# Kernel optimization log

Hardware: AMD Instinct MI355X
Metric: run time of the kernel (lower is better)

Reference implementation:

```python
import jax, jax.numpy as jnp
import numpy as np

N = 50000
E = 800000
F_IN = 128
HID = 32
C = 16


def setup_inputs() -> dict:
    key = jax.random.key(0)
    ks = jax.random.split(key, 8)
    x = jax.random.normal(ks[0], (N, F_IN), dtype=jnp.float32)
    edge_index = jax.random.randint(ks[1], (2, E), 0, N, dtype=jnp.int64)
    edge_attr = jax.random.uniform(ks[2], (E,), dtype=jnp.float32)
    W_rel1 = jax.random.normal(ks[3], (F_IN, HID), dtype=jnp.float32) / np.sqrt(F_IN)
    W_root1 = jax.random.normal(ks[4], (F_IN, HID), dtype=jnp.float32) / np.sqrt(F_IN)
    b1 = jnp.zeros((HID,), dtype=jnp.float32)
    W_rel2 = jax.random.normal(ks[5], (HID, C), dtype=jnp.float32) / np.sqrt(HID)
    W_root2 = jax.random.normal(ks[6], (HID, C), dtype=jnp.float32) / np.sqrt(HID)
    b2 = jnp.zeros((C,), dtype=jnp.float32)
    return {"x": x, "edge_index": edge_index, "edge_attr": edge_attr,
            "W_rel1": W_rel1, "W_root1": W_root1, "b1": b1,
            "W_rel2": W_rel2, "W_root2": W_root2, "b2": b2}


def reference(x, edge_index, edge_attr, W_rel1, W_root1, b1, W_rel2, W_root2, b2):
    src = edge_index[0]  # message source (x_j)
    dst = edge_index[1]  # aggregation target

    def graph_conv(h, W_rel, W_root, b):
        # PyG GraphConv: out = lin_rel(sum_{j in N(i)} w_ij * h_j) + lin_root(h_i)
        msg = h[src] * edge_attr[:, None]                       # [E, d]
        agg = jax.ops.segment_sum(msg, dst, num_segments=h.shape[0])  # [N, d]
        return agg @ W_rel + h @ W_root + b

    h = jax.nn.relu(graph_conv(x, W_rel1, W_root1, b1))          # [N, 32]
    out = graph_conv(h, W_rel2, W_root2, b2)                     # [N, C]
    return jax.nn.log_softmax(out, axis=1)
```

## Files before the change

### kernel.cpp

```cpp
#include <hip/hip_runtime.h>
#include <math.h>

#define N_NODES 50000
#define E_EDGES 800000
#define F_INDIM 128
#define HID 32
#define C_OUT 16

#define BSH 6
#define BNODE 64
#define NB 782
#define BCAP 1280
#define BINA_BLKS 128
#define CH 6250

#define K1ROWS 128
#define K1PAD 136
#define KC 32
#define K1BLKS 391

typedef unsigned long long u64;
typedef unsigned short ushort_t;

__device__ __forceinline__ ushort_t bf16rne(float f) {
    unsigned u = __float_as_uint(f);
    return (ushort_t)((u + 0x7FFFu + ((u >> 16) & 1u)) >> 16);
}
__device__ __forceinline__ float bf16tof(ushort_t b) {
    return __uint_as_float((unsigned)b << 16);
}

__global__ __launch_bounds__(512) void k_fuseA(
        const float* __restrict__ x,
        const float* __restrict__ Wrel, const float* __restrict__ Wroot,
        const float* __restrict__ b1,
        const int* __restrict__ ei, const float* __restrict__ ea,
        int* __restrict__ bcur, u64* __restrict__ arena,
        ushort_t* __restrict__ t1b, ushort_t* __restrict__ t2c) {
    __shared__ __align__(16) char smem[25600];
    const int tid = threadIdx.x;

    if (blockIdx.x < BINA_BLKS) {
        int* hist = (int*)smem;
        int* cur  = hist + NB;
        int* gb   = cur + NB;
        const int e0 = blockIdx.x * CH;

        for (int i = tid; i < NB; i += 512) hist[i] = 0;
        __syncthreads();
        for (int k = tid; k < CH; k += 512)
            atomicAdd(&hist[ei[E_EDGES + e0 + k] >> BSH], 1);
        __syncthreads();
        for (int i = tid; i < NB; i += 512) {
            int b = i + blockIdx.x; if (b >= NB) b -= NB;
            int cnt = hist[b];
            gb[b] = b * BCAP + (cnt ? atomicAdd(&bcur[b], cnt) : 0);
            cur[b] = 0;
        }
        __syncthreads();
        for (int k = tid; k < CH; k += 512) {
            int e = e0 + k;
            int src = ei[e];
            int dst = ei[E_EDGES + e];
            float w = ea[e];
            int bkt = dst >> BSH;
            int p = atomicAdd(&cur[bkt], 1);
            unsigned lo = (unsigned)src | ((unsigned)(dst & (BNODE - 1)) << 16);
            arena[(size_t)gb[bkt] + p] = (u64)lo | ((u64)__float_as_uint(w) << 32);
        }
    } else {
        float (*sW)[64] = (float(*)[64])smem;
        float (*sxT)[K1PAD] = (float(*)[K1PAD])(smem + 8192);
        const int rowBase = (blockIdx.x - BINA_BLKS) * K1ROWS;
        const int c = tid & 31;
        const int g = tid >> 5;
        const float4* x4 = (const float4*)x;

        float acc1[8], acc2[8];
#pragma unroll
        for (int i = 0; i < 8; ++i) { acc1[i] = 0.f; acc2[i] = 0.f; }

        for (int kc = 0; kc < F_INDIM / KC; ++kc) {
            const int k0 = kc * KC;
            for (int i = tid; i < KC * 64; i += 512) {
                int k = i >> 6, j = i & 63;
                int cc = j >> 1, m = j & 1;
                sW[k][j] = m ? Wroot[(k0 + k) * HID + cc]
                             : Wrel[(k0 + k) * HID + cc];
            }
            for (int i = tid; i < K1ROWS * (KC / 4); i += 512) {
                int r = i >> 3, q = i & 7;
                int row = rowBase + r;
                float4 v = make_float4(0.f, 0.f, 0.f, 0.f);
                if (row < N_NODES) v = x4[(size_t)row * 32 + (k0 >> 2) + q];
                sxT[4 * q + 0][r] = v.x;
                sxT[4 * q + 1][r] = v.y;
                sxT[4 * q + 2][r] = v.z;
                sxT[4 * q + 3][r] = v.w;
            }
            __syncthreads();
#pragma unroll 4
            for (int k = 0; k < KC; ++k) {
                float2 w = *(const float2*)&sW[k][2 * c];
                float4 xa = *(const float4*)&sxT[k][8 * g];
                float4 xb = *(const float4*)&sxT[k][8 * g + 4];
                acc1[0] = fmaf(xa.x, w.x, acc1[0]); acc2[0] = fmaf(xa.x, w.y, acc2[0]);
                acc1[1] = fmaf(xa.y, w.x, acc1[1]); acc2[1] = fmaf(xa.y, w.y, acc2[1]);
                acc1[2] = fmaf(xa.z, w.x, acc1[2]); acc2[2] = fmaf(xa.z, w.y, acc2[2]);
                acc1[3] = fmaf(xa.w, w.x, acc1[3]); acc2[3] = fmaf(xa.w, w.y, acc2[3]);
                acc1[4] = fmaf(xb.x, w.x, acc1[4]); acc2[4] = fmaf(xb.x, w.y, acc2[4]);
                acc1[5] = fmaf(xb.y, w.x, acc1[5]); acc2[5] = fmaf(xb.y, w.y, acc2[5]);
                acc1[6] = fmaf(xb.z, w.x, acc1[6]); acc2[6] = fmaf(xb.z, w.y, acc2[6]);
                acc1[7] = fmaf(xb.w, w.x, acc1[7]); acc2[7] = fmaf(xb.w, w.y, acc2[7]);
            }
            __syncthreads();
        }

        const float bc = b1[c];
#pragma unroll
        for (int i = 0; i < 8; ++i) {
            int row = rowBase + 8 * g + i;
            if (row < N_NODES) {
                t1b[(size_t)row * HID + c] = bf16rne(acc1[i]);
                t2c[(size_t)row * HID + c] = bf16rne(acc2[i] + bc);
            }
        }
    }
}

__global__ __launch_bounds__(256) void k_binB(const int* __restrict__ bcur,
                                              const u64* __restrict__ arena,
                                              unsigned* __restrict__ erec,
                                              int* __restrict__ rowptr) {
    __shared__ int cur[BNODE];
    __shared__ int hist[BNODE];
    __shared__ int sbase;
    const int tid = threadIdx.x;
    const int b = blockIdx.x;
    if (tid < 64) {
        int acc = 0;
        for (int i = tid; i < b; i += 64) acc += bcur[i];
#pragma unroll
        for (int d = 1; d < 64; d <<= 1) acc += __shfl_xor(acc, d);
        if (tid == 0) sbase = acc;
    }
    if (tid < BNODE) hist[tid] = 0;
    __syncthreads();
    const int cnt = bcur[b];
    const u64* seg = arena + (size_t)b * BCAP;
    for (int i = tid; i < cnt; i += 256)
        atomicAdd(&hist[((unsigned)seg[i] >> 16) & (BNODE - 1)], 1);
    __syncthreads();
    if (tid < 64) {
        int v = hist[tid];
        int inc = v;
#pragma unroll
        for (int d = 1; d < 64; d <<= 1) {
            int t = __shfl_up(inc, d);
            if (tid >= d) inc += t;
        }
        int ex = inc - v;
        cur[tid] = ex;
        int node = (b << BSH) + tid;
        if (node < N_NODES) rowptr[node] = sbase + ex;
    }
    if (b == NB - 1 && tid == 0) rowptr[N_NODES] = E_EDGES;
    __syncthreads();
    const int gbase = sbase;
    for (int i = tid; i < cnt; i += 256) {
        u64 r = seg[i];
        unsigned lo = (unsigned)r;
        int dl = (lo >> 16) & (BNODE - 1);
        int p = atomicAdd(&cur[dl], 1);
        unsigned wu = (unsigned)(r >> 32);
        unsigned wb = (wu + 0x7FFFu + ((wu >> 16) & 1u)) & 0xFFFF0000u;
        erec[gbase + p] = wb | (lo & 0xFFFFu);
    }
}

__global__ __launch_bounds__(256) void k_gather1(
        const int* __restrict__ rowptr, const unsigned* __restrict__ erec,
        const ushort_t* __restrict__ t1b, const ushort_t* __restrict__ t2c,
        const float* __restrict__ Wrel2, const float* __restrict__ Wroot2,
        const float* __restrict__ b2,
        ushort_t* __restrict__ u1b, float* __restrict__ u2b) {
    __shared__ float hbuf[4][HID];
    const int tid = threadIdx.x;
    const int lane = tid & 63;
    const int wid = tid >> 6;

    const int node = blockIdx.x * 4 + wid;
    const int start = rowptr[node];
    const int end = rowptr[node + 1];

    const int er2 = lane >> 5;
    const int j = lane & 31;
    const float* Wsel = (j < 16) ? (Wrel2 + (j & 15)) : (Wroot2 + (j & 15));
    float w2r[16];
#pragma unroll
    for (int kk = 0; kk < 16; ++kk)
        w2r[kk] = Wsel[(er2 * 16 + kk) * C_OUT];

    const int er = lane >> 3;
    const int c4 = lane & 7;
    float ax = 0.f, ay = 0.f, az = 0.f, aw = 0.f;
    float bx = 0.f, by = 0.f, bz = 0.f, bw = 0.f;
    int e = start + er;
    for (; e + 8 < end; e += 16) {
        unsigned r0 = erec[e];
        unsigned r1 = erec[e + 8];
        float w0 = __uint_as_float(r0 & 0xFFFF0000u);
        float w1 = __uint_as_float(r1 & 0xFFFF0000u);
        ushort4 p0 = *(const ushort4*)&t1b[(size_t)(r0 & 0xFFFFu) * HID + 4 * c4];
        ushort4 p1 = *(const ushort4*)&t1b[(size_t)(r1 & 0xFFFFu) * HID + 4 * c4];
        ax = fmaf(w0, bf16tof(p0.x), ax); ay = fmaf(w0, bf16tof(p0.y), ay);
        az = fmaf(w0, bf16tof(p0.z), az); aw = fmaf(w0, bf16tof(p0.w), aw);
        bx = fmaf(w1, bf16tof(p1.x), bx); by = fmaf(w1, bf16tof(p1.y), by);
        bz = fmaf(w1, bf16tof(p1.z), bz); bw = fmaf(w1, bf16tof(p1.w), bw);
    }
    if (e < end) {
        unsigned r0 = erec[e];
        float w0 = __uint_as_float(r0 & 0xFFFF0000u);
        ushort4 p0 = *(const ushort4*)&t1b[(size_t)(r0 & 0xFFFFu) * HID + 4 * c4];
        ax = fmaf(w0, bf16tof(p0.x), ax); ay = fmaf(w0, bf16tof(p0.y), ay);
        az = fmaf(w0, bf16tof(p0.z), az); aw = fmaf(w0, bf16tof(p0.w), aw);
    }
    ax += bx; ay += by; az += bz; aw += bw;
#pragma unroll
    for (int d = 8; d < 64; d <<= 1) {
        ax += __shfl_xor(ax, d);
        ay += __shfl_xor(ay, d);
        az += __shfl_xor(az, d);
        aw += __shfl_xor(aw, d);
    }
    ushort4 t2u = *(const ushort4*)&t2c[(size_t)node * HID + 4 * c4];
    float4 hv;
    hv.x = ax + bf16tof(t2u.x); hv.x = hv.x > 0.f ? hv.x : 0.f;
    hv.y = ay + bf16tof(t2u.y); hv.y = hv.y > 0.f ? hv.y : 0.f;
    hv.z = az + bf16tof(t2u.z); hv.z = hv.z > 0.f ? hv.z : 0.f;
    hv.w = aw + bf16tof(t2u.w); hv.w = hv.w > 0.f ? hv.w : 0.f;
    if (er == 0) *(float4*)&hbuf[wid][4 * c4] = hv;
    __syncthreads();

    float outv = 0.f;
#pragma unroll
    for (int kk = 0; kk < 16; ++kk)
        outv = fmaf(hbuf[wid][er2 * 16 + kk], w2r[kk], outv);
    outv += __shfl_xor(outv, 32);
    if (er2 == 0) {
        int cc = j & 15;
        if (j < 16) u1b[(size_t)node * C_OUT + cc] = bf16rne(outv);
        else        u2b[(size_t)node * C_OUT + cc] = outv + b2[cc];
    }
}

__global__ __launch_bounds__(256) void k_gather2(
        const int* __restrict__ rowptr, const unsigned* __restrict__ erec,
        const ushort_t* __restrict__ u1b, const float* __restrict__ u2b,
        float* __restrict__ out) {
    const int tid = threadIdx.x;
    const int lane = tid & 63;
    const int node = blockIdx.x * 4 + (tid >> 6);
    const int start = rowptr[node];
    const int end = rowptr[node + 1];
    const int er = lane >> 3;
    const int c2 = lane & 7;
    float a0x = 0.f, a0y = 0.f, a1x = 0.f, a1y = 0.f;
    int e = start + er;
    for (; e + 8 < end; e += 16) {
        unsigned r0 = erec[e];
        unsigned r1 = erec[e + 8];
        float w0 = __uint_as_float(r0 & 0xFFFF0000u);
        float w1 = __uint_as_float(r1 & 0xFFFF0000u);
        ushort2 p0 = *(const ushort2*)&u1b[(size_t)(r0 & 0xFFFFu) * C_OUT + 2 * c2];
        ushort2 p1 = *(const ushort2*)&u1b[(size_t)(r1 & 0xFFFFu) * C_OUT + 2 * c2];
        a0x = fmaf(w0, bf16tof(p0.x), a0x);
        a0y = fmaf(w0, bf16tof(p0.y), a0y);
        a1x = fmaf(w1, bf16tof(p1.x), a1x);
        a1y = fmaf(w1, bf16tof(p1.y), a1y);
    }
    if (e < end) {
        unsigned r0 = erec[e];
        float w0 = __uint_as_float(r0 & 0xFFFF0000u);
        ushort2 p0 = *(const ushort2*)&u1b[(size_t)(r0 & 0xFFFFu) * C_OUT + 2 * c2];
        a0x = fmaf(w0, bf16tof(p0.x), a0x);
        a0y = fmaf(w0, bf16tof(p0.y), a0y);
    }
    float ax = a0x + a1x;
    float ay = a0y + a1y;
    ax += __shfl_xor(ax, 8);  ay += __shfl_xor(ay, 8);
    ax += __shfl_xor(ax, 16); ay += __shfl_xor(ay, 16);
    ax += __shfl_xor(ax, 32); ay += __shfl_xor(ay, 32);
    float2 u2 = *(const float2*)&u2b[(size_t)node * C_OUT + 2 * c2];
    float vx = ax + u2.x;
    float vy = ay + u2.y;
    float mx = fmaxf(vx, vy);
#pragma unroll
    for (int d = 1; d < 8; d <<= 1) mx = fmaxf(mx, __shfl_xor(mx, d));
    float s = expf(vx - mx) + expf(vy - mx);
#pragma unroll
    for (int d = 1; d < 8; d <<= 1) s += __shfl_xor(s, d);
    float lse = mx + logf(s);
    if (er == 0)
        *(float2*)&out[(size_t)node * C_OUT + 2 * c2] = make_float2(vx - lse, vy - lse);
}

extern "C" void kernel_launch(void* const* d_in, const int* in_sizes, int n_in,
                              void* d_out, int out_size, void* d_ws, size_t ws_size,
                              hipStream_t stream) {
    const float* x      = (const float*)d_in[0];
    const int*   ei     = (const int*)d_in[1];
    const float* ea     = (const float*)d_in[2];
    const float* Wrel1  = (const float*)d_in[3];
    const float* Wroot1 = (const float*)d_in[4];
    const float* b1     = (const float*)d_in[5];
    const float* Wrel2  = (const float*)d_in[6];
    const float* Wroot2 = (const float*)d_in[7];
    const float* b2     = (const float*)d_in[8];
    float* out = (float*)d_out;

    float* ws = (float*)d_ws;
    float*    u2b  = ws;
    ushort_t* t1b  = (ushort_t*)(ws + 800000);
    ushort_t* t2c  = (ushort_t*)(ws + 1600000);
    ushort_t* u1b  = (ushort_t*)(ws + 2400000);
    u64*      arena = (u64*)(ws + 2600000);
    unsigned* erec = (unsigned*)(ws + 2600000 + (size_t)NB * BCAP * 2);
    int*      bcur   = (int*)(erec + E_EDGES);
    int*      rowptr = bcur + NB;

    (void)hipMemsetAsync(bcur, 0, NB * sizeof(int), stream);
    k_fuseA<<<BINA_BLKS + K1BLKS, 512, 0, stream>>>(
        x, Wrel1, Wroot1, b1, ei, ea, bcur, arena, t1b, t2c);
    k_binB<<<NB, 256, 0, stream>>>(bcur, arena, erec, rowptr);
    k_gather1<<<N_NODES / 4, 256, 0, stream>>>(
        rowptr, erec, t1b, t2c, Wrel2, Wroot2, b2, u1b, u2b);
    k_gather2<<<N_NODES / 4, 256, 0, stream>>>(rowptr, erec, u1b, u2b, out);
}
```

Baseline: 88.54 us.

## Fuse bin pass B into the first kernel using a global completion flag

Merges the second binning kernel into the fused first kernel as extra blocks. These blocks spin on a global counter until every bin-A block has signalled completion, then each one processes two buckets with its 512 threads. This removes one kernel launch and its boundary, and lets bin-B work overlap the dense GEMM blocks. It relies on the bin-A blocks being scheduled before or alongside the spinning blocks, so forward progress depends on block dispatch order, and spinning blocks can occupy CU slots.

After: 172.2 us. +94.5%, slower.

```diff
diff --git a/kernel.cpp b/kernel.cpp
--- a/kernel.cpp
+++ b/kernel.cpp
@@ -18,6 +18,8 @@
 #define K1PAD 136
 #define KC 32
 #define K1BLKS 391
+#define BINB_BLKS 391
+#define MEGA_BLKS (BINA_BLKS + K1BLKS + BINB_BLKS)
 
 typedef unsigned long long u64;
 typedef unsigned short ushort_t;
@@ -30,13 +32,15 @@
     return __uint_as_float((unsigned)b << 16);
 }
 
-__global__ __launch_bounds__(512) void k_fuseA(
+__global__ __launch_bounds__(512) void k_mega(
         const float* __restrict__ x,
         const float* __restrict__ Wrel, const float* __restrict__ Wroot,
         const float* __restrict__ b1,
         const int* __restrict__ ei, const float* __restrict__ ea,
-        int* __restrict__ bcur, u64* __restrict__ arena,
-        ushort_t* __restrict__ t1b, ushort_t* __restrict__ t2c) {
+        int* __restrict__ bcur, int* __restrict__ dflag,
+        u64* __restrict__ arena,
+        ushort_t* __restrict__ t1b, ushort_t* __restrict__ t2c,
+        unsigned* __restrict__ erec, int* __restrict__ rowptr) {
     __shared__ __align__(16) char smem[25600];
     const int tid = threadIdx.x;
 
@@ -68,7 +72,12 @@
             unsigned lo = (unsigned)src | ((unsigned)(dst & (BNODE - 1)) << 16);
             arena[(size_t)gb[bkt] + p] = (u64)lo | ((u64)__float_as_uint(w) << 32);
         }
-    } else {
+        __syncthreads();
+        if (tid == 0) {
+            __threadfence();
+            atomicAdd(dflag, 1);
+        }
+    } else if (blockIdx.x < BINA_BLKS + K1BLKS) {
         float (*sW)[64] = (float(*)[64])smem;
         float (*sxT)[K1PAD] = (float(*)[K1PAD])(smem + 8192);
         const int rowBase = (blockIdx.x - BINA_BLKS) * K1ROWS;
@@ -125,56 +134,62 @@
                 t2c[(size_t)row * HID + c] = bf16rne(acc2[i] + bc);
             }
         }
-    }
-}
-
-__global__ __launch_bounds__(256) void k_binB(const int* __restrict__ bcur,
-                                              const u64* __restrict__ arena,
-                                              unsigned* __restrict__ erec,
-                                              int* __restrict__ rowptr) {
-    __shared__ int cur[BNODE];
-    __shared__ int hist[BNODE];
-    __shared__ int sbase;
-    const int tid = threadIdx.x;
-    const int b = blockIdx.x;
-    if (tid < 64) {
-        int acc = 0;
-        for (int i = tid; i < b; i += 64) acc += bcur[i];
-#pragma unroll
-        for (int d = 1; d < 64; d <<= 1) acc += __shfl_xor(acc, d);
-        if (tid == 0) sbase = acc;
-    }
-    if (tid < BNODE) hist[tid] = 0;
-    __syncthreads();
-    const int cnt = bcur[b];
-    const u64* seg = arena + (size_t)b * BCAP;
-    for (int i = tid; i < cnt; i += 256)
-        atomicAdd(&hist[((unsigned)seg[i] >> 16) & (BNODE - 1)], 1);
-    __syncthreads();
-    if (tid < 64) {
-        int v = hist[tid];
-        int inc = v;
-#pragma unroll
-        for (int d = 1; d < 64; d <<= 1) {
-            int t = __shfl_up(inc, d);
-            if (tid >= d) inc += t;
-        }
-        int ex = inc - v;
-        cur[tid] = ex;
-        int node = (b << BSH) + tid;
-        if (node < N_NODES) rowptr[node] = sbase + ex;
-    }
-    if (b == NB - 1 && tid == 0) rowptr[N_NODES] = E_EDGES;
-    __syncthreads();
-    const int gbase = sbase;
-    for (int i = tid; i < cnt; i += 256) {
-        u64 r = seg[i];
-        unsigned lo = (unsigned)r;
-        int dl = (lo >> 16) & (BNODE - 1);
-        int p = atomicAdd(&cur[dl], 1);
-        unsigned wu = (unsigned)(r >> 32);
-        unsigned wb = (wu + 0x7FFFu + ((wu >> 16) & 1u)) & 0xFFFF0000u;
-        erec[gbase + p] = wb | (lo & 0xFFFFu);
+    } else {
+        int* hist2 = (int*)smem;
+        int* cur2  = hist2 + 2 * BNODE;
+        int* base2 = cur2 + 2 * BNODE;
+        if (tid == 0) {
+            while (atomicAdd(dflag, 0) < BINA_BLKS)
+                __builtin_amdgcn_s_sleep(2);
+        }
+        __syncthreads();
+        __threadfence();
+
+        const int half = tid >> 8;
+        const int ltid = tid & 255;
+        const int b = (blockIdx.x - (BINA_BLKS + K1BLKS)) * 2 + half;
+        int* hist = hist2 + half * BNODE;
+        int* cur  = cur2 + half * BNODE;
+
+        if (ltid < 64) {
+            int acc = 0;
+            for (int i = ltid; i < b; i += 64) acc += bcur[i];
+#pragma unroll
+            for (int d = 1; d < 64; d <<= 1) acc += __shfl_xor(acc, d);
+            if (ltid == 0) base2[half] = acc;
+        }
+        if (ltid < BNODE) hist[ltid] = 0;
+        __syncthreads();
+        const int cnt = bcur[b];
+        const u64* seg = arena + (size_t)b * BCAP;
+        for (int i = ltid; i < cnt; i += 256)
+            atomicAdd(&hist[((unsigned)seg[i] >> 16) & (BNODE - 1)], 1);
+        __syncthreads();
+        if (ltid < 64) {
+            int v = hist[ltid];
+            int inc = v;
+#pragma unroll
+            for (int d = 1; d < 64; d <<= 1) {
+                int t = __shfl_up(inc, d);
+                if (ltid >= d) inc += t;
+            }
+            int ex = inc - v;
+            cur[ltid] = ex;
+            int node = (b << BSH) + ltid;
+            if (node < N_NODES) rowptr[node] = base2[half] + ex;
+        }
+        if (b == NB - 1 && ltid == 0) rowptr[N_NODES] = E_EDGES;
+        __syncthreads();
+        const int gbase = base2[half];
+        for (int i = ltid; i < cnt; i += 256) {
+            u64 r = seg[i];
+            unsigned lo = (unsigned)r;
+            int dl = (lo >> 16) & (BNODE - 1);
+            int p = atomicAdd(&cur[dl], 1);
+            unsigned wu = (unsigned)(r >> 32);
+            unsigned wb = (wu + 0x7FFFu + ((wu >> 16) & 1u)) & 0xFFFF0000u;
+            erec[gbase + p] = wb | (lo & 0xFFFFu);
+        }
     }
 }
 
@@ -327,12 +342,12 @@
     u64*      arena = (u64*)(ws + 2600000);
     unsigned* erec = (unsigned*)(ws + 2600000 + (size_t)NB * BCAP * 2);
     int*      bcur   = (int*)(erec + E_EDGES);
-    int*      rowptr = bcur + NB;
-
-    (void)hipMemsetAsync(bcur, 0, NB * sizeof(int), stream);
-    k_fuseA<<<BINA_BLKS + K1BLKS, 512, 0, stream>>>(
-        x, Wrel1, Wroot1, b1, ei, ea, bcur, arena, t1b, t2c);
-    k_binB<<<NB, 256, 0, stream>>>(bcur, arena, erec, rowptr);
+    int*      dflag  = bcur + NB;
+    int*      rowptr = dflag + 1;
+
+    (void)hipMemsetAsync(bcur, 0, (NB + 1) * sizeof(int), stream);
+    k_mega<<<MEGA_BLKS, 512, 0, stream>>>(
+        x, Wrel1, Wroot1, b1, ei, ea, bcur, dflag, arena, t1b, t2c, erec, rowptr);
     k_gather1<<<N_NODES / 4, 256, 0, stream>>>(
         rowptr, erec, t1b, t2c, Wrel2, Wroot2, b2, u1b, u2b);
     k_gather2<<<N_NODES / 4, 256, 0, stream>>>(rowptr, erec, u1b, u2b, out);
```
